# Kernel optimization log

Measured on AMD Instinct MI355X. Metric: run time of the kernel, lower is better.

Reference implementation:

```python
import jax, jax.numpy as jnp
import numpy as np

TOPK = 2000        # post-score-sort candidates fed to NMS
NMS_THR = 0.5      # IOU suppression threshold


def get_iou(boxes1, boxes2):
    # boxes1: (A,4), boxes2: (B,4) in x1,y1,x2,y2 -> (A,B) IOU matrix
    area1 = (boxes1[:, 2] - boxes1[:, 0]) * (boxes1[:, 3] - boxes1[:, 1])
    area2 = (boxes2[:, 2] - boxes2[:, 0]) * (boxes2[:, 3] - boxes2[:, 1])
    lt = jnp.maximum(boxes1[:, None, :2], boxes2[None, :, :2])
    rb = jnp.minimum(boxes1[:, None, 2:], boxes2[None, :, 2:])
    wh = jnp.clip(rb - lt, 0.0)
    inter = wh[..., 0] * wh[..., 1]
    return inter / (area1[:, None] + area2[None, :] - inter)


def decode_boxes(box_transform_pred, boxes):
    # box_transform_pred: (N,C,4) dx,dy,dw,dh ; boxes: (N,4) -> (N,C,4)
    w = boxes[:, 2] - boxes[:, 0]
    h = boxes[:, 3] - boxes[:, 1]
    cx = boxes[:, 0] + 0.5 * w
    cy = boxes[:, 1] + 0.5 * h
    dx, dy, dw, dh = (box_transform_pred[..., i] for i in range(4))
    pcx = dx * w[:, None] + cx[:, None]
    pcy = dy * h[:, None] + cy[:, None]
    pw = jnp.exp(dw) * w[:, None]
    ph = jnp.exp(dh) * h[:, None]
    return jnp.stack((pcx - 0.5 * pw, pcy - 0.5 * ph,
                      pcx + 0.5 * pw, pcy + 0.5 * ph), axis=2)


def encode_boxes(gt, boxes):
    # boxes_to_transformation_targets: (N,4),(N,4) -> (N,4) tx,ty,tw,th
    w = boxes[:, 2] - boxes[:, 0]
    h = boxes[:, 3] - boxes[:, 1]
    cx = boxes[:, 0] + 0.5 * w
    cy = boxes[:, 1] + 0.5 * h
    gw = gt[:, 2] - gt[:, 0]
    gh = gt[:, 3] - gt[:, 1]
    gcx = gt[:, 0] + 0.5 * gw
    gcy = gt[:, 1] + 0.5 * gh
    return jnp.stack(((gcx - cx) / w, (gcy - cy) / h,
                      jnp.log(gw / w), jnp.log(gh / h)), axis=1)


def clamp_boxes(boxes, h, w):
    x1 = jnp.clip(boxes[..., 0], 0.0, w)
    y1 = jnp.clip(boxes[..., 1], 0.0, h)
    x2 = jnp.clip(boxes[..., 2], 0.0, w)
    y2 = jnp.clip(boxes[..., 3], 0.0, h)
    return jnp.stack((x1, y1, x2, y2), axis=-1)


def nms_keep(iou_kk, thr):
    # greedy NMS over score-sorted boxes; sequential via lax.scan
    K = iou_kk.shape[0]
    idx = jnp.arange(K)
    def step(suppressed, i):
        keep_i = ~suppressed[i]
        suppressed = suppressed | (keep_i & (iou_kk[i] > thr) & (idx > i))
        return suppressed, keep_i
    _, keep = jax.lax.scan(step, jnp.zeros((K,), bool), idx)
    return keep


def _make_boxes(key, n, h, w):
    k1, k2, k3, k4 = jax.random.split(key, 4)
    x1 = jax.random.uniform(k1, (n,)) * (w - 128.0)
    y1 = jax.random.uniform(k2, (n,)) * (h - 128.0)
    bw = jax.random.uniform(k3, (n,)) * 120.0 + 4.0
    bh = jax.random.uniform(k4, (n,)) * 120.0 + 4.0
    return jnp.stack((x1, y1, x1 + bw, y1 + bh), axis=1)


def setup_inputs() -> dict:
    key = jax.random.key(0)
    N, C, G, H, W = 200000, 21, 128, 800, 1333
    k1, k2, k3, k4 = jax.random.split(key, 4)
    return {
        "proposals": _make_boxes(k1, N, H, W),
        "box_transform_pred": jax.random.normal(k2, (N, C, 4)) * 0.1,
        "cls_scores": jax.random.normal(k3, (N, C)),
        "gt_boxes": _make_boxes(k4, G, H, W),
        "image_h": H,
        "image_w": W,
    }


def reference(proposals, box_transform_pred, cls_scores, gt_boxes, image_h, image_w):
    h = float(image_h); w = float(image_w)
    N = proposals.shape[0]
    # 1. decode all per-class boxes and clamp to image boundary  (N,C,4)
    pred_boxes = clamp_boxes(decode_boxes(box_transform_pred, proposals), h, w)
    iou = get_iou(gt_boxes, proposals)          # (G,N)
    best_idx = jnp.argmax(iou, axis=0)          # (N,)
    matched_gt = gt_boxes[best_idx]             # (N,4)
    reg_targets = encode_boxes(matched_gt, proposals)  # (N,4)
    # 3. per-proposal best foreground class score/box
    probs = jax.nn.softmax(cls_scores, axis=-1)
    fg = probs[:, 1:]
    score = jnp.max(fg, axis=-1)                # (N,)
    cls = jnp.argmax(fg, axis=-1) + 1           # (N,)
    idx = jnp.broadcast_to(cls[:, None, None], (N, 1, 4))
    box_per = jnp.take_along_axis(pred_boxes, idx, axis=1)[:, 0]  # (N,4)
    # 4. top-K by score, greedy NMS
    top_scores, top_idx = jax.lax.top_k(score, TOPK)
    top_boxes = box_per[top_idx]                # (K,4)
    keep = nms_keep(get_iou(top_boxes, top_boxes), NMS_THR)
    final = top_boxes * keep[:, None].astype(top_boxes.dtype)  # suppressed zeroed
    return jnp.concatenate([final, reg_targets], axis=0)
```

## Files before the change

kernel.cpp:

```cpp
#include <hip/hip_runtime.h>
#include <cstdint>

#define TOPK 2000
#define NMS_THR 0.5f
#define NCLS 21
#define HSHIFT 14
#define HBINS (1u << 16)
#define NCHUNK 256
#define CAND_CAP 4096
#define TPAD 2048

typedef unsigned long long u64;
typedef unsigned int u32;
typedef float f32x4 __attribute__((ext_vector_type(4)));

__device__ __forceinline__ u32 hperm(u32 bin) { return ((bin & 255u) << 8) | (bin >> 8); }

__device__ __forceinline__ float iou_pair(float ax1, float ay1, float ax2, float ay2, float aarea,
                                          float bx1, float by1, float bx2, float by2, float barea) {
#pragma clang fp contract(off)
    float ltx = fmaxf(ax1, bx1), lty = fmaxf(ay1, by1);
    float rbx = fminf(ax2, bx2), rby = fminf(ay2, by2);
    float wx = fmaxf(rbx - ltx, 0.f), wy = fmaxf(rby - lty, 0.f);
    float inter = wx * wy;
    return inter / (aarea + barea - inter);
}

__global__ __launch_bounds__(256) void k_prep(const float* __restrict__ cls,
                                              float* __restrict__ clsT,
                                              u32* __restrict__ hist, u32* __restrict__ csum,
                                              u32* __restrict__ meta, u32* __restrict__ rank,
                                              int N) {
    __shared__ float slds[256 * NCLS];
    int b = blockIdx.x, t = threadIdx.x;

    for (int v = b * 256 + t; v < (int)(HBINS / 4); v += gridDim.x * 256)
        ((uint4*)hist)[v] = make_uint4(0u, 0u, 0u, 0u);
    if (b == 0) {
        csum[t] = 0u;
        if (t < 64) meta[t] = 0u;
    }
    if (b < 16) rank[b * 256 + t] = 0u;

    int row0 = b * 256;
    int rows = N - row0;
    if (rows <= 0) return;
    if (rows > 256) rows = 256;
    if (rows == 256) {
        const uint4* __restrict__ src = (const uint4*)(cls + (size_t)row0 * NCLS);
        uint4* __restrict__ dst = (uint4*)slds;
        for (int v = t; v < 1344; v += 256) dst[v] = src[v];
    } else {
        int nw = rows * NCLS;
        const float* __restrict__ src = cls + (size_t)row0 * NCLS;
        for (int v = t; v < nw; v += 256) slds[v] = src[v];
    }
    __syncthreads();
    if (t < rows) {
#pragma unroll
        for (int c = 0; c < NCLS; ++c)
            clsT[(size_t)c * N + row0 + t] = slds[t * NCLS + c];
    }
}

__global__ __launch_bounds__(256, 3) void k_main(
    const float* __restrict__ prop, const float* __restrict__ btp,
    const float* __restrict__ clsT, const float* __restrict__ gt,
    const int* __restrict__ hptr, const int* __restrict__ wptr,
    float* __restrict__ out, float4* __restrict__ box_per,
    u32* __restrict__ score_bits, u32* __restrict__ hist,
    int N, int G) {
#pragma clang fp contract(off)
    __shared__ float4 sgt[256];
    __shared__ float sga[256];
    int tid = threadIdx.x;
    for (int g = tid; g < G; g += 256) {
        float4 gb = ((const float4*)gt)[g];
        sgt[g] = gb;
        sga[g] = (gb.z - gb.x) * (gb.w - gb.y);
    }
    __syncthreads();

    int i = blockIdx.x * 256 + tid;
    if (i >= N) return;

    float W = (float)wptr[0], H = (float)hptr[0];
    float4 p = ((const float4*)prop)[i];
    float pw = p.z - p.x, ph = p.w - p.y;
    float pcx = p.x + 0.5f * pw, pcy = p.y + 0.5f * ph;

    float e[NCLS];
#pragma unroll
    for (int c = 0; c < NCLS; ++c) e[c] = clsT[(size_t)c * N + i];

    float m = e[0];
#pragma unroll
    for (int c = 1; c < NCLS; ++c) m = fmaxf(m, e[c]);
#pragma unroll
    for (int c = 0; c < NCLS; ++c) e[c] = expf(e[c] - m);
    float Z = 0.f;
#pragma unroll
    for (int c = 0; c < NCLS; ++c) Z += e[c];
    float best = -1.f;
    int bc = 1;
#pragma unroll
    for (int c = 1; c < NCLS; ++c) {
        float pr = e[c] / Z;
        if (pr > best) { best = pr; bc = c; }
    }

    float4 t = ((const float4*)btp)[(size_t)i * NCLS + bc];

    u32 b = __float_as_uint(best);
    score_bits[i] = b;
    atomicAdd(&hist[hperm(b >> HSHIFT)], 1u);

    float parea = pw * ph;
    float bestiou = -1.f;
    int bi = 0;
    int g = 0;
    for (; g + 8 <= G; g += 8) {
        float4 g0 = sgt[g], g1 = sgt[g + 1], g2 = sgt[g + 2], g3 = sgt[g + 3];
        float4 g4 = sgt[g + 4], g5 = sgt[g + 5], g6 = sgt[g + 6], g7 = sgt[g + 7];
        float a0 = sga[g], a1 = sga[g + 1], a2 = sga[g + 2], a3 = sga[g + 3];
        float a4 = sga[g + 4], a5 = sga[g + 5], a6 = sga[g + 6], a7 = sga[g + 7];
        float v0 = iou_pair(g0.x, g0.y, g0.z, g0.w, a0, p.x, p.y, p.z, p.w, parea);
        float v1 = iou_pair(g1.x, g1.y, g1.z, g1.w, a1, p.x, p.y, p.z, p.w, parea);
        float v2 = iou_pair(g2.x, g2.y, g2.z, g2.w, a2, p.x, p.y, p.z, p.w, parea);
        float v3 = iou_pair(g3.x, g3.y, g3.z, g3.w, a3, p.x, p.y, p.z, p.w, parea);
        float v4 = iou_pair(g4.x, g4.y, g4.z, g4.w, a4, p.x, p.y, p.z, p.w, parea);
        float v5 = iou_pair(g5.x, g5.y, g5.z, g5.w, a5, p.x, p.y, p.z, p.w, parea);
        float v6 = iou_pair(g6.x, g6.y, g6.z, g6.w, a6, p.x, p.y, p.z, p.w, parea);
        float v7 = iou_pair(g7.x, g7.y, g7.z, g7.w, a7, p.x, p.y, p.z, p.w, parea);
        float va = v0; int ia = g;
        if (v1 > va) { va = v1; ia = g + 1; }
        float vb = v2; int ib = g + 2;
        if (v3 > vb) { vb = v3; ib = g + 3; }
        if (vb > va) { va = vb; ia = ib; }
        float vc = v4; int ic = g + 4;
        if (v5 > vc) { vc = v5; ic = g + 5; }
        float vd = v6; int id_ = g + 6;
        if (v7 > vd) { vd = v7; id_ = g + 7; }
        if (vd > vc) { vc = vd; ic = id_; }
        if (vc > va) { va = vc; ia = ic; }
        if (va > bestiou) { bestiou = va; bi = ia; }
    }
    for (; g < G; ++g) {
        float4 gb = sgt[g];
        float v = iou_pair(gb.x, gb.y, gb.z, gb.w, sga[g], p.x, p.y, p.z, p.w, parea);
        if (v > bestiou) { bestiou = v; bi = g; }
    }

    float qcx = t.x * pw + pcx, qcy = t.y * ph + pcy;
    float qw = expf(t.z) * pw, qh = expf(t.w) * ph;
    float bx1 = fminf(fmaxf(qcx - 0.5f * qw, 0.f), W);
    float by1 = fminf(fmaxf(qcy - 0.5f * qh, 0.f), H);
    float bx2 = fminf(fmaxf(qcx + 0.5f * qw, 0.f), W);
    float by2 = fminf(fmaxf(qcy + 0.5f * qh, 0.f), H);
    f32x4 bp = {bx1, by1, bx2, by2};
    __builtin_nontemporal_store(bp, (f32x4*)&box_per[i]);

    float4 mg = sgt[bi];
    float gw = mg.z - mg.x, gh = mg.w - mg.y;
    float gcx = mg.x + 0.5f * gw, gcy = mg.y + 0.5f * gh;
    f32x4 rt = {(gcx - pcx) / pw, (gcy - pcy) / ph, logf(gw / pw), logf(gh / ph)};
    __builtin_nontemporal_store(rt, (f32x4*)(out + 4 * (size_t)(TOPK + i)));
}

__global__ __launch_bounds__(256) void k_hsum_scan(const u32* __restrict__ hist,
                                                   u32* __restrict__ csum,
                                                   u32* __restrict__ meta) {
    __shared__ u32 ps[4];
    __shared__ u32 S[NCHUNK];
    __shared__ u32 sh_tc, sh_E;
    __shared__ int slast;
    int b = blockIdx.x, t = threadIdx.x;

    u32 v = hist[(size_t)t * 256 + b];
#pragma unroll
    for (int o = 32; o; o >>= 1) v += __shfl_xor(v, o);
    if ((t & 63) == 0) ps[t >> 6] = v;
    __syncthreads();
    if (t == 0) {
        u32 tot = ps[0] + ps[1] + ps[2] + ps[3];
        atomicAdd(&csum[b], tot);
        __threadfence();
        u32 old = atomicAdd(&meta[62], 1u);
        slast = (old == NCHUNK - 1u) ? 1 : 0;
    }
    __syncthreads();
    if (!slast) return;

    u32 c = atomicAdd(&csum[t], 0u);
    S[t] = c;
    __syncthreads();
    for (int off = 1; off < NCHUNK; off <<= 1) {
        u32 x = (t + off < NCHUNK) ? S[t + off] : 0u;
        __syncthreads();
        S[t] += x;
        __syncthreads();
    }
    u32 suff = S[t];
    u32 E = suff - c;
    if (suff >= TOPK && E < TOPK) { sh_tc = (u32)t; sh_E = E; }
    __syncthreads();
    u32 tc = sh_tc, E0 = sh_E;
    u32 hh = hist[(size_t)t * 256 + tc];
    __syncthreads();
    S[t] = hh;
    __syncthreads();
    for (int off = 1; off < NCHUNK; off <<= 1) {
        u32 x = (t + off < NCHUNK) ? S[t + off] : 0u;
        __syncthreads();
        S[t] += x;
        __syncthreads();
    }
    u32 tot2 = E0 + S[t];
    if (tot2 >= TOPK && (tot2 - hh) < TOPK) meta[0] = tc * 256u + (u32)t;
}

__global__ __launch_bounds__(256) void k_compact(const u32* __restrict__ score_bits,
                                                 const u32* __restrict__ meta, u32* __restrict__ cnt,
                                                 u64* __restrict__ keys, int N) {
    int i = blockIdx.x * 256 + threadIdx.x;
    if (i >= N) return;
    u32 b = score_bits[i];
    if ((b >> HSHIFT) >= meta[0]) {
        u32 pos = atomicAdd(cnt, 1u);
        if (pos < CAND_CAP) keys[pos] = ((u64)b << 32) | (u32)(~(u32)i);
    }
}

__global__ __launch_bounds__(256) void k_rank1(const u64* __restrict__ keys,
                                               const u32* __restrict__ meta,
                                               u32* __restrict__ rank) {
    __shared__ u64 sk[256];
    int it = blockIdx.x & 15, js = blockIdx.x >> 4;
    int t = threadIdx.x;
    u32 M = meta[1];
    if (M > CAND_CAP) M = CAND_CAP;
    u32 Mp = (M + 63u) & ~63u;
    u32 j0 = (u32)js * 256u;
    if (j0 >= Mp) return;
    u32 jn = Mp - j0; if (jn > 256u) jn = 256u;
    sk[t] = ((u32)t < jn && j0 + t < M) ? keys[j0 + t] : 0ull;
    __syncthreads();
    int idx = it * 256 + t;
    u64 k = (idx < (int)M) ? keys[idx] : ~0ull;
    u32 r = 0;
    int lane = t & 63;
    for (u32 jj = 0; jj < jn; jj += 64) {
        u64 tv = sk[jj + lane];
        u32 tlo = (u32)tv, thi = (u32)(tv >> 32);
#pragma unroll
        for (int l = 0; l < 64; ++l) {
            u64 kj = ((u64)(u32)__builtin_amdgcn_readlane(thi, l) << 32) |
                     (u64)(u32)__builtin_amdgcn_readlane(tlo, l);
            r += (kj > k) ? 1u : 0u;
        }
    }
    if (idx < (int)M && r) atomicAdd(&rank[idx], r);
}

__global__ __launch_bounds__(256) void k_rank2(const u64* __restrict__ keys,
                                               const u32* __restrict__ meta,
                                               const u32* __restrict__ rank,
                                               const float4* __restrict__ box_per,
                                               float4* __restrict__ topbox) {
    int idx = blockIdx.x * 256 + threadIdx.x;
    u32 M = meta[1];
    if (M > CAND_CAP) M = CAND_CAP;
    if (idx >= (int)M) return;
    u32 r = rank[idx];
    if (r < TOPK) {
        u64 k = keys[idx];
        topbox[r] = box_per[~(u32)(k & 0xffffffffull)];
    }
}

__global__ __launch_bounds__(256) void k_mask(const float4* __restrict__ topbox,
                                              u64* __restrict__ mask) {
#pragma clang fp contract(off)
    int gid = blockIdx.x * 256 + threadIdx.x;
    int w = gid >> 11, i = gid & (TPAD - 1);
    u64 m = 0;
    int j0 = w << 6;
    if (i < TOPK && j0 + 63 > i) {
        float4 a = topbox[i];
        float aarea = (a.z - a.x) * (a.w - a.y);
        for (int jj = 0; jj < 64; ++jj) {
            int j = j0 + jj;
            if (j < TOPK && j > i) {
                float4 b = topbox[j];
                float barea = (b.z - b.x) * (b.w - b.y);
                float v = iou_pair(a.x, a.y, a.z, a.w, aarea, b.x, b.y, b.z, b.w, barea);
                if (v > NMS_THR) m |= (1ull << jj);
            }
        }
    }
    mask[(size_t)i * 32 + w] = m;
}

__global__ __launch_bounds__(256) void k_nms(const u64* __restrict__ mask,
                                             const float4* __restrict__ topbox,
                                             float* __restrict__ out) {
    __shared__ u64 sm[2][64 * 32];
    __shared__ u64 srem[32];
    int t = threadIdx.x;
    int lane = t & 63;
    u32 lw = (u32)(lane & 31);
    u32 rlo = 0, rhi = 0;

    {
        const uint4* __restrict__ src = (const uint4*)mask;
        uint4 v0 = src[t], v1 = src[t + 256], v2 = src[t + 512], v3 = src[t + 768];
        uint4* __restrict__ dst = (uint4*)sm[0];
        dst[t] = v0; dst[t + 256] = v1; dst[t + 512] = v2; dst[t + 768] = v3;
    }
    __syncthreads();

    for (int c = 0; c < 32; ++c) {
        if (t >= 64 && t < 192) {
            if (c + 1 < 32) {
                const uint4* __restrict__ src = (const uint4*)(mask + (size_t)(c + 1) * 2048);
                uint4* __restrict__ dst = (uint4*)sm[(c + 1) & 1];
                int u = t - 64;
                uint4 v0 = src[u];
                uint4 v1 = src[u + 128];
                uint4 v2 = src[u + 256];
                uint4 v3 = src[u + 384];
                uint4 v4 = src[u + 512];
                uint4 v5 = src[u + 640];
                uint4 v6 = src[u + 768];
                uint4 v7 = src[u + 896];
                dst[u] = v0;
                dst[u + 128] = v1;
                dst[u + 256] = v2;
                dst[u + 384] = v3;
                dst[u + 512] = v4;
                dst[u + 640] = v5;
                dst[u + 768] = v6;
                dst[u + 896] = v7;
            }
        } else if (t < 64) {
            const u64* __restrict__ buf = sm[c & 1];
            u32 d_lo = (u32)__builtin_amdgcn_readlane(rlo, c);
            u32 d_hi = (u32)__builtin_amdgcn_readlane(rhi, c);
            u64 ring[8], dring[8];
#pragma unroll
            for (int p = 0; p < 8; ++p) {
                ring[p] = buf[p * 32 + lw];
                dring[p] = buf[p * 32 + c];
            }
#pragma unroll
            for (int l = 0; l < 64; ++l) {
                u64 row = ring[l & 7];
                u64 dg = dring[l & 7];
                if (l < 56) {
                    ring[l & 7] = buf[(l + 8) * 32 + lw];
                    dring[l & 7] = buf[(l + 8) * 32 + c];
                }
                u32 sc_lo = (u32)dg, sc_hi = (u32)(dg >> 32);
                u32 bit = (l < 32) ? ((d_lo >> l) & 1u) : ((d_hi >> (l - 32)) & 1u);
                u32 mk = bit - 1u;
                d_lo |= sc_lo & mk;
                d_hi |= sc_hi & mk;
                rlo |= (u32)row & mk;
                rhi |= (u32)(row >> 32) & mk;
            }
        }
        __syncthreads();
    }
    if (t < 32) srem[t] = ((u64)rhi << 32) | rlo;
    __syncthreads();
    for (int r = t; r < TOPK; r += 256) {
        bool sup = (srem[r >> 6] >> (r & 63)) & 1ull;
        float4 b = topbox[r];
        ((float4*)out)[r] = sup ? make_float4(0.f, 0.f, 0.f, 0.f) : b;
    }
}

extern "C" void kernel_launch(void* const* d_in, const int* in_sizes, int n_in,
                              void* d_out, int out_size, void* d_ws, size_t ws_size,
                              hipStream_t stream) {
    const float* prop = (const float*)d_in[0];
    const float* btp = (const float*)d_in[1];
    const float* cls = (const float*)d_in[2];
    const float* gt = (const float*)d_in[3];
    const int* hptr = (const int*)d_in[4];
    const int* wptr = (const int*)d_in[5];
    float* out = (float*)d_out;
    int N = in_sizes[0] / 4;
    int G = in_sizes[3] / 4;
    if (G > 256) G = 256;

    char* ws = (char*)d_ws;
    size_t o = 0;
    u32* hist = (u32*)(ws + o);       o += (size_t)HBINS * 4;
    u32* csum = (u32*)(ws + o);       o += NCHUNK * 4;
    u32* meta = (u32*)(ws + o);       o += 256;
    u32* rank = (u32*)(ws + o);       o += (size_t)CAND_CAP * 4;
    u32* score_bits = (u32*)(ws + o); o += (((size_t)N * 4 + 255) & ~(size_t)255);
    u64* keys = (u64*)(ws + o);       o += (size_t)CAND_CAP * 8;
    float4* box_per = (float4*)(ws + o); o += (size_t)N * 16;
    float4* topbox = (float4*)(ws + o);  o += (size_t)TPAD * 16;
    u64* mask = (u64*)(ws + o);       o += (size_t)TPAD * 32 * 8;
    float* clsT = (float*)(ws + o);   o += (size_t)N * NCLS * 4;
    (void)o; (void)ws_size; (void)n_in; (void)out_size;

    int nb = (N + 255) / 256;
    k_prep<<<nb, 256, 0, stream>>>(cls, clsT, hist, csum, meta, rank, N);
    k_main<<<nb, 256, 0, stream>>>(prop, btp, clsT, gt, hptr, wptr, out, box_per, score_bits,
                                   hist, N, G);
    k_hsum_scan<<<NCHUNK, 256, 0, stream>>>(hist, csum, meta);
    k_compact<<<nb, 256, 0, stream>>>(score_bits, meta, meta + 1, keys, N);
    k_rank1<<<256, 256, 0, stream>>>(keys, meta, rank);
    k_rank2<<<CAND_CAP / 256, 256, 0, stream>>>(keys, meta, rank, box_per, topbox);
    k_mask<<<(32 * TPAD) / 256, 256, 0, stream>>>(topbox, mask);
    k_nms<<<1, 256, 0, stream>>>(mask, topbox, out);
}
```

Measured before the change: 236.7 us.

## Split each proposal across two threads in k_main for GT IOU argmax

Each proposal is now handled by a pair of threads. Each thread scans alternate ground-truth boxes for the best IOU, and the pair merges its results with a shuffle that breaks ties toward the lower index. The decode and box-store work goes to one thread of the pair, and the score, histogram and regression-target work goes to the other. Launch bounds rise to 6 waves and the grid doubles. This halves the serial G-loop per thread and raises parallelism, at the cost of both threads recomputing the softmax and loading the class scores twice.

```diff
diff --git a/kernel.cpp b/kernel.cpp
--- a/kernel.cpp
+++ b/kernel.cpp
@@ -63,7 +63,7 @@
     }
 }
 
-__global__ __launch_bounds__(256, 3) void k_main(
+__global__ __launch_bounds__(256, 6) void k_main(
     const float* __restrict__ prop, const float* __restrict__ btp,
     const float* __restrict__ clsT, const float* __restrict__ gt,
     const int* __restrict__ hptr, const int* __restrict__ wptr,
@@ -81,7 +81,8 @@
     }
     __syncthreads();
 
-    int i = blockIdx.x * 256 + tid;
+    int h = tid & 1;
+    int i = blockIdx.x * 128 + (tid >> 1);
     if (i >= N) return;
 
     float W = (float)wptr[0], H = (float)hptr[0];
@@ -92,7 +93,6 @@
     float e[NCLS];
 #pragma unroll
     for (int c = 0; c < NCLS; ++c) e[c] = clsT[(size_t)c * N + i];
-
     float m = e[0];
 #pragma unroll
     for (int c = 1; c < NCLS; ++c) m = fmaxf(m, e[c]);
@@ -109,62 +109,73 @@
         if (pr > best) { best = pr; bc = c; }
     }
 
-    float4 t = ((const float4*)btp)[(size_t)i * NCLS + bc];
-
-    u32 b = __float_as_uint(best);
-    score_bits[i] = b;
-    atomicAdd(&hist[hperm(b >> HSHIFT)], 1u);
+    float4 t = make_float4(0.f, 0.f, 0.f, 0.f);
+    if (h) {
+        t = ((const float4*)btp)[(size_t)i * NCLS + bc];
+    } else {
+        u32 b = __float_as_uint(best);
+        score_bits[i] = b;
+        atomicAdd(&hist[hperm(b >> HSHIFT)], 1u);
+    }
 
     float parea = pw * ph;
     float bestiou = -1.f;
     int bi = 0;
-    int g = 0;
-    for (; g + 8 <= G; g += 8) {
-        float4 g0 = sgt[g], g1 = sgt[g + 1], g2 = sgt[g + 2], g3 = sgt[g + 3];
-        float4 g4 = sgt[g + 4], g5 = sgt[g + 5], g6 = sgt[g + 6], g7 = sgt[g + 7];
-        float a0 = sga[g], a1 = sga[g + 1], a2 = sga[g + 2], a3 = sga[g + 3];
-        float a4 = sga[g + 4], a5 = sga[g + 5], a6 = sga[g + 6], a7 = sga[g + 7];
-        float v0 = iou_pair(g0.x, g0.y, g0.z, g0.w, a0, p.x, p.y, p.z, p.w, parea);
-        float v1 = iou_pair(g1.x, g1.y, g1.z, g1.w, a1, p.x, p.y, p.z, p.w, parea);
-        float v2 = iou_pair(g2.x, g2.y, g2.z, g2.w, a2, p.x, p.y, p.z, p.w, parea);
-        float v3 = iou_pair(g3.x, g3.y, g3.z, g3.w, a3, p.x, p.y, p.z, p.w, parea);
-        float v4 = iou_pair(g4.x, g4.y, g4.z, g4.w, a4, p.x, p.y, p.z, p.w, parea);
-        float v5 = iou_pair(g5.x, g5.y, g5.z, g5.w, a5, p.x, p.y, p.z, p.w, parea);
-        float v6 = iou_pair(g6.x, g6.y, g6.z, g6.w, a6, p.x, p.y, p.z, p.w, parea);
-        float v7 = iou_pair(g7.x, g7.y, g7.z, g7.w, a7, p.x, p.y, p.z, p.w, parea);
+    int g = h;
+    for (; g + 14 < G; g += 16) {
+        float4 q0 = sgt[g], q1 = sgt[g + 2], q2 = sgt[g + 4], q3 = sgt[g + 6];
+        float4 q4 = sgt[g + 8], q5 = sgt[g + 10], q6 = sgt[g + 12], q7 = sgt[g + 14];
+        float a0 = sga[g], a1 = sga[g + 2], a2 = sga[g + 4], a3 = sga[g + 6];
+        float a4 = sga[g + 8], a5 = sga[g + 10], a6 = sga[g + 12], a7 = sga[g + 14];
+        float v0 = iou_pair(q0.x, q0.y, q0.z, q0.w, a0, p.x, p.y, p.z, p.w, parea);
+        float v1 = iou_pair(q1.x, q1.y, q1.z, q1.w, a1, p.x, p.y, p.z, p.w, parea);
+        float v2 = iou_pair(q2.x, q2.y, q2.z, q2.w, a2, p.x, p.y, p.z, p.w, parea);
+        float v3 = iou_pair(q3.x, q3.y, q3.z, q3.w, a3, p.x, p.y, p.z, p.w, parea);
+        float v4 = iou_pair(q4.x, q4.y, q4.z, q4.w, a4, p.x, p.y, p.z, p.w, parea);
+        float v5 = iou_pair(q5.x, q5.y, q5.z, q5.w, a5, p.x, p.y, p.z, p.w, parea);
+        float v6 = iou_pair(q6.x, q6.y, q6.z, q6.w, a6, p.x, p.y, p.z, p.w, parea);
+        float v7 = iou_pair(q7.x, q7.y, q7.z, q7.w, a7, p.x, p.y, p.z, p.w, parea);
         float va = v0; int ia = g;
-        if (v1 > va) { va = v1; ia = g + 1; }
-        float vb = v2; int ib = g + 2;
-        if (v3 > vb) { vb = v3; ib = g + 3; }
+        if (v1 > va) { va = v1; ia = g + 2; }
+        float vb = v2; int ib = g + 4;
+        if (v3 > vb) { vb = v3; ib = g + 6; }
         if (vb > va) { va = vb; ia = ib; }
-        float vc = v4; int ic = g + 4;
-        if (v5 > vc) { vc = v5; ic = g + 5; }
-        float vd = v6; int id_ = g + 6;
-        if (v7 > vd) { vd = v7; id_ = g + 7; }
+        float vc = v4; int ic = g + 8;
+        if (v5 > vc) { vc = v5; ic = g + 10; }
+        float vd = v6; int id_ = g + 12;
+        if (v7 > vd) { vd = v7; id_ = g + 14; }
         if (vd > vc) { vc = vd; ic = id_; }
         if (vc > va) { va = vc; ia = ic; }
         if (va > bestiou) { bestiou = va; bi = ia; }
     }
-    for (; g < G; ++g) {
+    for (; g < G; g += 2) {
         float4 gb = sgt[g];
         float v = iou_pair(gb.x, gb.y, gb.z, gb.w, sga[g], p.x, p.y, p.z, p.w, parea);
         if (v > bestiou) { bestiou = v; bi = g; }
     }
 
-    float qcx = t.x * pw + pcx, qcy = t.y * ph + pcy;
-    float qw = expf(t.z) * pw, qh = expf(t.w) * ph;
-    float bx1 = fminf(fmaxf(qcx - 0.5f * qw, 0.f), W);
-    float by1 = fminf(fmaxf(qcy - 0.5f * qh, 0.f), H);
-    float bx2 = fminf(fmaxf(qcx + 0.5f * qw, 0.f), W);
-    float by2 = fminf(fmaxf(qcy + 0.5f * qh, 0.f), H);
-    f32x4 bp = {bx1, by1, bx2, by2};
-    __builtin_nontemporal_store(bp, (f32x4*)&box_per[i]);
-
-    float4 mg = sgt[bi];
-    float gw = mg.z - mg.x, gh = mg.w - mg.y;
-    float gcx = mg.x + 0.5f * gw, gcy = mg.y + 0.5f * gh;
-    f32x4 rt = {(gcx - pcx) / pw, (gcy - pcy) / ph, logf(gw / pw), logf(gh / ph)};
-    __builtin_nontemporal_store(rt, (f32x4*)(out + 4 * (size_t)(TOPK + i)));
+    float vp = __shfl_xor(bestiou, 1);
+    int ip = __shfl_xor(bi, 1);
+    float ve = h ? vp : bestiou;  int ie = h ? ip : bi;
+    float vO = h ? bestiou : vp;  int iO = h ? bi : ip;
+    int ifin = (vO > ve || (vO == ve && iO < ie)) ? iO : ie;
+
+    if (h) {
+        float qcx = t.x * pw + pcx, qcy = t.y * ph + pcy;
+        float qw = expf(t.z) * pw, qh = expf(t.w) * ph;
+        float bx1 = fminf(fmaxf(qcx - 0.5f * qw, 0.f), W);
+        float by1 = fminf(fmaxf(qcy - 0.5f * qh, 0.f), H);
+        float bx2 = fminf(fmaxf(qcx + 0.5f * qw, 0.f), W);
+        float by2 = fminf(fmaxf(qcy + 0.5f * qh, 0.f), H);
+        f32x4 bp = {bx1, by1, bx2, by2};
+        __builtin_nontemporal_store(bp, (f32x4*)&box_per[i]);
+    } else {
+        float4 mg = sgt[ifin];
+        float gw = mg.z - mg.x, gh = mg.w - mg.y;
+        float gcx = mg.x + 0.5f * gw, gcy = mg.y + 0.5f * gh;
+        f32x4 rt = {(gcx - pcx) / pw, (gcy - pcy) / ph, logf(gw / pw), logf(gh / ph)};
+        __builtin_nontemporal_store(rt, (f32x4*)(out + 4 * (size_t)(TOPK + i)));
+    }
 }
 
 __global__ __launch_bounds__(256) void k_hsum_scan(const u32* __restrict__ hist,
@@ -408,12 +419,12 @@
     float* clsT = (float*)(ws + o);   o += (size_t)N * NCLS * 4;
     (void)o; (void)ws_size; (void)n_in; (void)out_size;
 
-    int nb = (N + 255) / 256;
-    k_prep<<<nb, 256, 0, stream>>>(cls, clsT, hist, csum, meta, rank, N);
-    k_main<<<nb, 256, 0, stream>>>(prop, btp, clsT, gt, hptr, wptr, out, box_per, score_bits,
-                                   hist, N, G);
+    int nb256 = (N + 255) / 256;
+    k_prep<<<nb256, 256, 0, stream>>>(cls, clsT, hist, csum, meta, rank, N);
+    k_main<<<(N + 127) / 128, 256, 0, stream>>>(prop, btp, clsT, gt, hptr, wptr, out,
+                                                box_per, score_bits, hist, N, G);
     k_hsum_scan<<<NCHUNK, 256, 0, stream>>>(hist, csum, meta);
-    k_compact<<<nb, 256, 0, stream>>>(score_bits, meta, meta + 1, keys, N);
+    k_compact<<<nb256, 256, 0, stream>>>(score_bits, meta, meta + 1, keys, N);
     k_rank1<<<256, 256, 0, stream>>>(keys, meta, rank);
     k_rank2<<<CAND_CAP / 256, 256, 0, stream>>>(keys, meta, rank, box_per, topbox);
     k_mask<<<(32 * TPAD) / 256, 256, 0, stream>>>(topbox, mask);
```

Result: no change. 237.0 us (+0.1%).
